# Performance work log

Measured on AMD Instinct MI355X. Metric: run time of the kernel, lower is better.

The kernel has to match this reference:

```python
import jax, jax.numpy as jnp
import numpy as np

B, T, D = 4, 2048, 768
D_CONV, D_GRIF, D_FFN, K = 384, 384, 2048, 3
EPS = 1e-6


def rmsnorm(x, w):
    rms = jax.lax.rsqrt(jnp.mean(jnp.square(x.astype(jnp.float32)), axis=-1, keepdims=True) + EPS)
    return (x.astype(jnp.float32) * rms).astype(x.dtype) * w


def causal_dwconv(x, w):
    # x: [B,T,C], w: [C,K] depthwise causal conv
    k = w.shape[1]
    xp = jnp.pad(x, ((0, 0), (k - 1, 0), (0, 0)))  # left pad -> causal
    out = jax.lax.conv_general_dilated(
        xp.transpose(0, 2, 1), w[:, None, :],  # [B,C,T+K-1], [C,1,K]
        window_strides=(1,), padding='VALID',
        dimension_numbers=('NCW', 'OIW', 'NCW'),
        feature_group_count=w.shape[0])
    return out.transpose(0, 2, 1)  # [B,T,C]


def rg_lru(v, r, i, lam):
    # Griffin RG-LRU: log_a = -8*softplus(lam)*r; h_t = a*h_{t-1} + sqrt(1-a^2)*(i*v)
    log_a = -8.0 * jax.nn.softplus(lam) * r                # [B,T,Dg]
    a = jnp.exp(log_a)
    gated = jnp.sqrt(jnp.maximum(1.0 - jnp.exp(2.0 * log_a), EPS)) * (i * v)
    def comb(c1, c2):
        a1, b1 = c1
        a2, b2 = c2
        return (a1 * a2, a2 * b1 + b2)
    _, h = jax.lax.associative_scan(comb, (a, gated), axis=1)
    return h


def setup_inputs() -> dict:
    key = jax.random.key(0)
    ks = jax.random.split(key, 16)
    s_in = 1.0 / np.sqrt(D)
    s_ffn = 1.0 / np.sqrt(D_FFN)
    return {
        'x': jax.random.normal(ks[0], (B, T, D), jnp.float32),
        'velocity': jnp.zeros((B, T, D), jnp.float32),
        'pre_norm_w': jnp.ones((D,), jnp.float32),
        'conv_in_w': jax.random.normal(ks[1], (D, 2 * D_CONV), jnp.float32) * s_in,
        'conv_dw_w': jax.random.normal(ks[2], (D_CONV, K), jnp.float32) * (1.0 / np.sqrt(K)),
        'grif_v_w': jax.random.normal(ks[3], (D, D_GRIF), jnp.float32) * s_in,
        'grif_r_w': jax.random.normal(ks[4], (D, D_GRIF), jnp.float32) * s_in,
        'grif_i_w': jax.random.normal(ks[5], (D, D_GRIF), jnp.float32) * s_in,
        'grif_lam': jax.random.uniform(ks[6], (D_GRIF,), jnp.float32, 0.5, 2.0),
        'out_w': jax.random.normal(ks[7], (D, D), jnp.float32) * s_in,
        'log_beta': jnp.array(0.0, jnp.float32),  # log(0.5/(1-0.5))
        'ffn_norm_w': jnp.ones((D,), jnp.float32),
        'w1': jax.random.normal(ks[8], (D, D_FFN), jnp.float32) * s_in,
        'w3': jax.random.normal(ks[9], (D, D_FFN), jnp.float32) * s_in,
        'w2': jax.random.normal(ks[10], (D_FFN, D), jnp.float32) * s_ffn,
    }


def reference(x, velocity, pre_norm_w, conv_in_w, conv_dw_w, grif_v_w, grif_r_w,
              grif_i_w, grif_lam, out_w, log_beta, ffn_norm_w, w1, w3, w2):
    xn = rmsnorm(x, pre_norm_w)
    # GatedConv branch -> [B,T,D_CONV]
    u, g = jnp.split(xn @ conv_in_w, 2, axis=-1)
    conv_out = causal_dwconv(u, conv_dw_w) * jax.nn.silu(g)
    # Griffin RG-LRU branch -> [B,T,D_GRIF]
    v = xn @ grif_v_w
    r = jax.nn.sigmoid(xn @ grif_r_w)
    i = jax.nn.sigmoid(xn @ grif_i_w)
    griffin_out = rg_lru(v, r, i, grif_lam)
    # concat -> out_proj -> momentum residual
    mixer_out = jnp.concatenate([conv_out, griffin_out], axis=-1) @ out_w
    beta = jax.nn.sigmoid(log_beta)
    velocity = beta * velocity + mixer_out
    x = x + velocity
    # ffn: RMSNorm -> SwiGLU -> residual
    normed = rmsnorm(x, ffn_norm_w)
    x = x + (jax.nn.silu(normed @ w1) * (normed @ w3)) @ w2
    return (x, velocity)
```

## Files before the change

kernel.cpp:

```cpp
#include <hip/hip_runtime.h>
#include <hip/hip_bf16.h>
#include <cstdint>

#define BSZ   4
#define TSEQ  2048
#define DMOD  768
#define DCONV 384
#define DGRIF 384
#define DFFN  2048
#define BT    (BSZ*TSEQ)
#define NG1   1920
#define EPS_  1e-6f

typedef __bf16 bf16;
typedef __bf16 bf16x8 __attribute__((ext_vector_type(8)));
typedef float  f32x4  __attribute__((ext_vector_type(4)));

__device__ __forceinline__ float sigmoidf_(float x) { return 1.f / (1.f + __expf(-x)); }

__device__ __forceinline__ void gload_lds16(const void* g, void* l) {
  __builtin_amdgcn_global_load_lds(
      (const __attribute__((address_space(1))) void*)(uintptr_t)g,
      (__attribute__((address_space(3))) void*)(uint32_t)(uintptr_t)l,
      16, 0, 0);
}

__device__ __forceinline__ int swz_wg() {
  const int nwg = gridDim.x;
  const int bid = blockIdx.x;
  const int cpx = nwg >> 3;
  return (bid & 7) * cpx + (bid >> 3);
}

__global__ __launch_bounds__(256) void prep_kernel(
    const float* __restrict__ conv_in_w, const float* __restrict__ gv,
    const float* __restrict__ gr, const float* __restrict__ gi,
    const float* __restrict__ out_w, const float* __restrict__ w1,
    const float* __restrict__ w3, const float* __restrict__ w2,
    bf16* __restrict__ WT_G1, bf16* __restrict__ WT_OUT,
    bf16* __restrict__ WT_W13, bf16* __restrict__ WT_W2,
    const float* __restrict__ x, const float* __restrict__ pre_w,
    bf16* __restrict__ XN)
{
  __shared__ float tile[32][33];
  if (blockIdx.x >= 6624) {
    const int row = blockIdx.x - 6624;
    const int tid = threadIdx.x;
    const float* xr = x + (size_t)row * DMOD;
    float v0 = xr[tid], v1 = xr[tid + 256], v2 = xr[tid + 512];
    float s = v0*v0 + v1*v1 + v2*v2;
    #pragma unroll
    for (int o = 32; o > 0; o >>= 1) s += __shfl_down(s, o, 64);
    __shared__ float sbuf[4];
    if ((tid & 63) == 0) sbuf[tid >> 6] = s;
    __syncthreads();
    float tot = sbuf[0] + sbuf[1] + sbuf[2] + sbuf[3];
    float rms = rsqrtf(tot * (1.f / (float)DMOD) + EPS_);
    bf16* orow = XN + (size_t)row * DMOD;
    orow[tid]       = (bf16)(v0 * rms * pre_w[tid]);
    orow[tid + 256] = (bf16)(v1 * rms * pre_w[tid + 256]);
    orow[tid + 512] = (bf16)(v2 * rms * pre_w[tid + 512]);
    return;
  }
  int t = blockIdx.x;
  const float* W; bf16* Wt; int R, C, mode = 0, half = 0;
  if      (t < 576)  {           W = conv_in_w; Wt = WT_G1;                        R = 768;  C = 768; }
  else if (t < 864)  { t -= 576;  W = gv;  Wt = WT_G1 + (size_t)768  * DMOD;       R = 768;  C = 384; }
  else if (t < 1152) { t -= 864;  W = gr;  Wt = WT_G1 + (size_t)1152 * DMOD;       R = 768;  C = 384; }
  else if (t < 1440) { t -= 1152; W = gi;  Wt = WT_G1 + (size_t)1536 * DMOD;       R = 768;  C = 384; }
  else if (t < 2016) { t -= 1440; W = out_w; Wt = WT_OUT;                          R = 768;  C = 768; }
  else if (t < 3552) { t -= 2016; W = w1;  Wt = WT_W13; mode = 1; half = 0;        R = 768;  C = 2048; }
  else if (t < 5088) { t -= 3552; W = w3;  Wt = WT_W13; mode = 1; half = 64;       R = 768;  C = 2048; }
  else               { t -= 5088; W = w2;  Wt = WT_W2;                             R = 2048; C = 768; }

  const int xt = C >> 5;
  const int tc = (t % xt) * 32, tr = (t / xt) * 32;
  const int lx = threadIdx.x & 31;
  const int ly = threadIdx.x >> 5;
  #pragma unroll
  for (int i = ly; i < 32; i += 8) {
    int r = tr + i, c = tc + lx;
    tile[i][lx] = (r < R && c < C) ? W[(size_t)r * C + c] : 0.f;
  }
  __syncthreads();
  #pragma unroll
  for (int i = ly; i < 32; i += 8) {
    int oc = tc + i;
    int orr = tr + lx;
    if (oc < C && orr < R) {
      int orow = (mode == 0) ? oc : ((oc >> 6) << 7) + half + (oc & 63);
      Wt[(size_t)orow * R + orr] = (bf16)tile[lx][i];
    }
  }
}

__global__ __launch_bounds__(256) void rmsnorm_kernel(
    const float* __restrict__ x, const float* __restrict__ w, bf16* __restrict__ out)
{
  __shared__ float sbuf[4];
  const int row = blockIdx.x;
  const int tid = threadIdx.x;
  const float* xr = x + (size_t)row * DMOD;
  float v0 = xr[tid], v1 = xr[tid + 256], v2 = xr[tid + 512];
  float s = v0*v0 + v1*v1 + v2*v2;
  #pragma unroll
  for (int o = 32; o > 0; o >>= 1) s += __shfl_down(s, o, 64);
  if ((tid & 63) == 0) sbuf[tid >> 6] = s;
  __syncthreads();
  float tot = sbuf[0] + sbuf[1] + sbuf[2] + sbuf[3];
  float rms = rsqrtf(tot * (1.f / (float)DMOD) + EPS_);
  bf16* orow = out + (size_t)row * DMOD;
  orow[tid]       = (bf16)(v0 * rms * w[tid]);
  orow[tid + 256] = (bf16)(v1 * rms * w[tid + 256]);
  orow[tid + 512] = (bf16)(v2 * rms * w[tid + 512]);
}

__global__ __launch_bounds__(256) void gemm_w128(
    const bf16* __restrict__ A, const bf16* __restrict__ Bt, bf16* __restrict__ C,
    int M, int N, int K, int nx)
{
  __shared__ alignas(16) unsigned short As[128 * 64];
  __shared__ alignas(16) unsigned short Bs[128 * 64];

  const int wg = swz_wg();
  const int m0 = (wg / nx) * 128, n0 = (wg % nx) * 128;
  const int tid  = threadIdx.x;
  const int wave = tid >> 6;
  const int lane = tid & 63;
  const int wr = wave >> 1, wc = wave & 1;

  f32x4 acc[4][4] = {};
  const int srow = lane >> 3;
  const int scol = ((lane & 7) ^ srow) * 8;
  const int lr = lane & 15;
  const int lsw = lr & 7;
  const int lk4 = lane >> 4;

  for (int k0 = 0; k0 < K; k0 += 64) {
    __syncthreads();
    #pragma unroll
    for (int it = 0; it < 4; ++it) {
      const int chunk = wave * 4 + it;
      const int row = chunk * 8 + srow;
      gload_lds16(A  + (size_t)(m0 + row) * K + k0 + scol, (char*)As + chunk * 1024);
      gload_lds16(Bt + (size_t)(n0 + row) * K + k0 + scol, (char*)Bs + chunk * 1024);
    }
    __syncthreads();
    #pragma unroll
    for (int kk = 0; kk < 2; ++kk) {
      bf16x8 af[4], bfr[4];
      #pragma unroll
      for (int i = 0; i < 4; ++i)
        af[i] = *reinterpret_cast<const bf16x8*>(
            &As[(wr*64 + i*16 + lr) * 64 + (((kk*4 + lk4) ^ lsw) * 8)]);
      #pragma unroll
      for (int i = 0; i < 4; ++i)
        bfr[i] = *reinterpret_cast<const bf16x8*>(
            &Bs[(wc*64 + i*16 + lr) * 64 + (((kk*4 + lk4) ^ lsw) * 8)]);
      #pragma unroll
      for (int mi = 0; mi < 4; ++mi)
        #pragma unroll
        for (int ni = 0; ni < 4; ++ni)
          acc[mi][ni] = __builtin_amdgcn_mfma_f32_16x16x32_bf16(af[mi], bfr[ni], acc[mi][ni], 0, 0, 0);
    }
  }

  #pragma unroll
  for (int mi = 0; mi < 4; ++mi)
    #pragma unroll
    for (int ni = 0; ni < 4; ++ni)
      #pragma unroll
      for (int reg = 0; reg < 4; ++reg) {
        const int r = m0 + wr*64 + mi*16 + lk4 * 4 + reg;
        const int c = n0 + wc*64 + ni*16 + lr;
        C[(size_t)r * N + c] = (bf16)acc[mi][ni][reg];
      }
}

__global__ __launch_bounds__(512) void gemm_ffn13b(
    const bf16* __restrict__ A, const bf16* __restrict__ Bt, bf16* __restrict__ H,
    int M, int K)
{
  __shared__ alignas(16) unsigned short As[256 * 64];
  __shared__ alignas(16) unsigned short Bs[128 * 64];
  bf16* comb = reinterpret_cast<bf16*>(As);

  const int xcd = blockIdx.x & 7;
  const int w   = blockIdx.x >> 3;
  const int mt  = (xcd & 3) * 8 + (w >> 4);
  const int bx  = (xcd >> 2) * 16 + (w & 15);
  const int m0 = mt * 256;
  const int n0 = bx * 128;
  const int tid  = threadIdx.x;
  const int wave = tid >> 6;
  const int lane = tid & 63;
  const int wr = wave >> 1;
  const int wc = wave & 1;
  const int lr = lane & 15;
  const int lk4 = lane >> 4;

  f32x4 acc[4][4] = {};

  for (int k0 = 0; k0 < K; k0 += 64) {
    __syncthreads();
    #pragma unroll
    for (int p = 0; p < 4; ++p) {
      const int f = (p << 9) + tid;
      const int row = f >> 3;
      const int gs = (f & 7) ^ (row & 7);
      gload_lds16(A + (size_t)(m0 + row) * K + k0 + gs * 8,
                  (char*)As + (p << 13) + (wave << 10));
    }
    #pragma unroll
    for (int p = 0; p < 2; ++p) {
      const int f = (p << 9) + tid;
      const int row = f >> 3;
      const int gs = (f & 7) ^ (row & 7);
      gload_lds16(Bt + (size_t)(n0 + row) * K + k0 + gs * 8,
                  (char*)Bs + (p << 13) + (wave << 10));
    }
    __syncthreads();
    #pragma unroll
    for (int kk = 0; kk < 2; ++kk) {
      bf16x8 af[4], bfr[4];
      #pragma unroll
      for (int i = 0; i < 4; ++i) {
        const int r = wr*64 + i*16 + lr;
        af[i] = *reinterpret_cast<const bf16x8*>(&As[r * 64 + (((kk*4 + lk4) ^ (r & 7)) * 8)]);
      }
      #pragma unroll
      for (int i = 0; i < 4; ++i) {
        const int r = wc*64 + i*16 + lr;
        bfr[i] = *reinterpret_cast<const bf16x8*>(&Bs[r * 64 + (((kk*4 + lk4) ^ (r & 7)) * 8)]);
      }
      #pragma unroll
      for (int mi = 0; mi < 4; ++mi)
        #pragma unroll
        for (int ni = 0; ni < 4; ++ni)
          acc[mi][ni] = __builtin_amdgcn_mfma_f32_16x16x32_bf16(af[mi], bfr[ni], acc[mi][ni], 0, 0, 0);
    }
  }

  __syncthreads();
  if (wc == 1) {
    #pragma unroll
    for (int mi = 0; mi < 4; ++mi)
      #pragma unroll
      for (int ni = 0; ni < 4; ++ni)
        #pragma unroll
        for (int reg = 0; reg < 4; ++reg) {
          const int row = wr*64 + mi*16 + lk4 * 4 + reg;
          const int col = ni*16 + lr;
          comb[row * 64 + col] = (bf16)acc[mi][ni][reg];
        }
  }
  __syncthreads();
  if (wc == 0) {
    #pragma unroll
    for (int mi = 0; mi < 4; ++mi)
      #pragma unroll
      for (int ni = 0; ni < 4; ++ni)
        #pragma unroll
        for (int reg = 0; reg < 4; ++reg) {
          const int row = wr*64 + mi*16 + lk4 * 4 + reg;
          const int col = ni*16 + lr;
          float p3 = (float)comb[row * 64 + col];
          float p1 = acc[mi][ni][reg];
          H[(size_t)(m0 + row) * DFFN + bx * 64 + col] = (bf16)(p1 * sigmoidf_(p1) * p3);
        }
  }
}

template <int EPI>
__global__ __launch_bounds__(256) void gemm_n64(
    const bf16* __restrict__ A, const bf16* __restrict__ Bt, float* __restrict__ C,
    const float* __restrict__ xin, const float* __restrict__ vin,
    float* __restrict__ outv, const float* __restrict__ log_beta,
    int M, int N, int K, int nx)
{
  __shared__ alignas(16) unsigned short As[2][128 * 64];
  __shared__ alignas(16) unsigned short Bs[2][64 * 64];

  const int wg = swz_wg();
  const int m0 = (wg / nx) * 128, n0 = (wg % nx) * 64;
  const int tid  = threadIdx.x;
  const int wave = tid >> 6;
  const int lane = tid & 63;
  const int wr = wave >> 1, wc = wave & 1;

  f32x4 acc[4][2] = {};
  const int srow = lane >> 3;
  const int scol = ((lane & 7) ^ srow) * 8;
  const int lr = lane & 15;
  const int lsw = lr & 7;
  const int lk4 = lane >> 4;

  auto stage = [&](int buf, int k0) {
    #pragma unroll
    for (int it = 0; it < 6; ++it) {
      const int chunk = wave * 6 + it;
      if (chunk < 16) {
        const int row = chunk * 8 + srow;
        gload_lds16(A + (size_t)(m0 + row) * K + k0 + scol,
                    (char*)As[buf] + chunk * 1024);
      } else {
        const int row = (chunk - 16) * 8 + srow;
        gload_lds16(Bt + (size_t)(n0 + row) * K + k0 + scol,
                    (char*)Bs[buf] + (chunk - 16) * 1024);
      }
    }
  };

  stage(0, 0);
  __syncthreads();

  int cur = 0;
  for (int k0 = 0; k0 < K; k0 += 64) {
    if (k0 + 64 < K) stage(cur ^ 1, k0 + 64);
    #pragma unroll
    for (int kk = 0; kk < 2; ++kk) {
      bf16x8 af[4], bfr[2];
      #pragma unroll
      for (int i = 0; i < 4; ++i)
        af[i] = *reinterpret_cast<const bf16x8*>(
            &As[cur][(wr*64 + i*16 + lr) * 64 + (((kk*4 + lk4) ^ lsw) * 8)]);
      #pragma unroll
      for (int i = 0; i < 2; ++i)
        bfr[i] = *reinterpret_cast<const bf16x8*>(
            &Bs[cur][(wc*32 + i*16 + lr) * 64 + (((kk*4 + lk4) ^ lsw) * 8)]);
      #pragma unroll
      for (int mi = 0; mi < 4; ++mi)
        #pragma unroll
        for (int ni = 0; ni < 2; ++ni)
          acc[mi][ni] = __builtin_amdgcn_mfma_f32_16x16x32_bf16(af[mi], bfr[ni], acc[mi][ni], 0, 0, 0);
    }
    __syncthreads();
    cur ^= 1;
  }

  const float beta = (EPI == 0) ? sigmoidf_(log_beta[0]) : 0.f;
  #pragma unroll
  for (int mi = 0; mi < 4; ++mi)
    #pragma unroll
    for (int ni = 0; ni < 2; ++ni)
      #pragma unroll
      for (int reg = 0; reg < 4; ++reg) {
        const int r = m0 + wr*64 + mi*16 + lk4 * 4 + reg;
        const int c = n0 + wc*32 + ni*16 + lr;
        const size_t off = (size_t)r * N + c;
        float v = acc[mi][ni][reg];
        if (EPI == 0) {
          float vel = beta * vin[off] + v;
          float x1  = xin[off] + vel;
          outv[off] = vel;
          C[off] = x1;
        } else {
          C[off] += v;
        }
      }
}

#define NCH  32
#define CLEN 64

__device__ __forceinline__ void lru_step(const bf16* row, int c, float coef,
                                         float& a, float& g)
{
  float v  = (float)row[2*DCONV + c];
  float r  = sigmoidf_((float)row[2*DCONV + DGRIF + c]);
  float is = sigmoidf_((float)row[2*DCONV + 2*DGRIF + c]);
  float la = coef * r;
  a = __expf(la);
  g = sqrtf(fmaxf(1.f - __expf(2.f * la), EPS_)) * (is * v);
}

__global__ __launch_bounds__(256) void lru_pass1(
    const bf16* __restrict__ g1, const float* __restrict__ lam,
    float* __restrict__ cA, float* __restrict__ cB)
{
  const int idx = blockIdx.x * 256 + threadIdx.x;
  const int c = idx % DGRIF;
  const int rest = idx / DGRIF;
  const int j = rest & (NCH - 1);
  const int b = rest / NCH;
  const float coef = -8.f * log1pf(__expf(lam[c]));
  const bf16* base = g1 + (size_t)(b * TSEQ + j * CLEN) * NG1;
  float A = 1.f, Bv = 0.f;
  #pragma unroll 4
  for (int t = 0; t < CLEN; ++t) {
    float a, g;
    lru_step(base + (size_t)t * NG1, c, coef, a, g);
    A *= a;
    Bv = a * Bv + g;
  }
  cA[((size_t)b * DGRIF + c) * NCH + j] = A;
  cB[((size_t)b * DGRIF + c) * NCH + j] = Bv;
}

__global__ __launch_bounds__(256) void lru_pass2(
    const bf16* __restrict__ g1, const float* __restrict__ lam,
    const float* __restrict__ cA, const float* __restrict__ cB,
    const float* __restrict__ dw, bf16* __restrict__ mixin)
{
  const int idx = blockIdx.x * 256 + threadIdx.x;
  const int c = idx % DGRIF;
  const int rest = idx / DGRIF;
  const int j = rest & (NCH - 1);
  const int b = rest / NCH;
  const float coef = -8.f * log1pf(__expf(lam[c]));
  float Hc = 0.f;
  const float* pa = cA + ((size_t)b * DGRIF + c) * NCH;
  const float* pb = cB + ((size_t)b * DGRIF + c) * NCH;
  for (int k = 0; k < j; ++k) Hc = pa[k] * Hc + pb[k];

  const int t0 = j * CLEN;
  const bf16* base = g1 + (size_t)(b * TSEQ + t0) * NG1;
  const float w0 = dw[c*3], w1 = dw[c*3 + 1], w2 = dw[c*3 + 2];
  float u1 = (t0 >= 1) ? (float)base[-(ptrdiff_t)NG1 + c]     : 0.f;
  float u0 = (t0 >= 2) ? (float)base[-(ptrdiff_t)(2*NG1) + c] : 0.f;

  bf16* mbase = mixin + (size_t)(b * TSEQ + t0) * DMOD;
  #pragma unroll 4
  for (int t = 0; t < CLEN; ++t) {
    const bf16* row = base + (size_t)t * NG1;
    float u2 = (float)row[c];
    float gg = (float)row[DCONV + c];
    float conv = u0 * w0 + u1 * w1 + u2 * w2;
    mbase[(size_t)t * DMOD + c] = (bf16)(conv * (gg * sigmoidf_(gg)));
    u0 = u1; u1 = u2;
    float a, g;
    lru_step(row, c, coef, a, g);
    Hc = a * Hc + g;
    mbase[(size_t)t * DMOD + DCONV + c] = (bf16)Hc;
  }
}

extern "C" void kernel_launch(void* const* d_in, const int* in_sizes, int n_in,
                              void* d_out, int out_size, void* d_ws, size_t ws_size,
                              hipStream_t stream)
{
  const float* x         = (const float*)d_in[0];
  const float* vel_in    = (const float*)d_in[1];
  const float* pre_w     = (const float*)d_in[2];
  const float* conv_in_w = (const float*)d_in[3];
  const float* conv_dw   = (const float*)d_in[4];
  const float* gv        = (const float*)d_in[5];
  const float* gr        = (const float*)d_in[6];
  const float* gi        = (const float*)d_in[7];
  const float* lam       = (const float*)d_in[8];
  const float* out_w     = (const float*)d_in[9];
  const float* log_beta  = (const float*)d_in[10];
  const float* ffn_w     = (const float*)d_in[11];
  const float* w1        = (const float*)d_in[12];
  const float* w3        = (const float*)d_in[13];
  const float* w2        = (const float*)d_in[14];

  char* ws = (char*)d_ws;
  size_t off = 0;
  auto alloc = [&](size_t bytes) { void* p = ws + off; off += (bytes + 255) & ~(size_t)255; return p; };

  bf16*  WT_G1  = (bf16*)alloc((size_t)NG1 * DMOD * 2);
  bf16*  WT_OUT = (bf16*)alloc((size_t)DMOD * DMOD * 2);
  bf16*  WT_W13 = (bf16*)alloc((size_t)2 * DFFN * DMOD * 2);
  bf16*  WT_W2  = (bf16*)alloc((size_t)DMOD * DFFN * 2);
  float* CA     = (float*)alloc((size_t)BSZ * DGRIF * NCH * 4);
  float* CB     = (float*)alloc((size_t)BSZ * DGRIF * NCH * 4);
  bf16*  XN     = (bf16*)alloc((size_t)BT * DMOD * 2);
  bf16*  G1     = (bf16*)alloc((size_t)BT * NG1 * 2);
  bf16*  MIXIN  = (bf16*)alloc((size_t)BT * DMOD * 2);
  bf16*  H      = (bf16*)alloc((size_t)BT * DFFN * 2);
  bf16*  NORMED = (bf16*)alloc((size_t)BT * DMOD * 2);

  float* OUTX   = (float*)d_out;
  float* OUTV   = OUTX + (size_t)BT * DMOD;

  prep_kernel<<<6624 + BT, 256, 0, stream>>>(conv_in_w, gv, gr, gi, out_w, w1, w3, w2,
                                             WT_G1, WT_OUT, WT_W13, WT_W2,
                                             x, pre_w, XN);

  gemm_w128<<<(NG1/128) * (BT/128), 256, 0, stream>>>(XN, WT_G1, G1, BT, NG1, DMOD, NG1/128);

  lru_pass1<<<(BSZ * NCH * DGRIF) / 256, 256, 0, stream>>>(G1, lam, CA, CB);
  lru_pass2<<<(BSZ * NCH * DGRIF) / 256, 256, 0, stream>>>(G1, lam, CA, CB, conv_dw, MIXIN);

  gemm_n64<0><<<(DMOD/64) * (BT/128), 256, 0, stream>>>(MIXIN, WT_OUT, OUTX, x, vel_in, OUTV,
                                                        log_beta, BT, DMOD, DMOD, DMOD/64);

  rmsnorm_kernel<<<BT, 256, 0, stream>>>(OUTX, ffn_w, NORMED);

  gemm_ffn13b<<<(BT/256) * (DFFN/64), 512, 0, stream>>>(NORMED, WT_W13, H, BT, DMOD);

  gemm_n64<1><<<(DMOD/64) * (BT/128), 256, 0, stream>>>(H, WT_W2, OUTX, nullptr, nullptr, nullptr,
                                                        nullptr, BT, DMOD, DFFN, DMOD/64);
}
```

Measured before the change: 259.9 us.

## Double-buffer LDS in input and FFN up-projection GEMMs, shrink FFN tile

Both the first projection GEMM and the fused W1/W3 GEMM now use two LDS buffers, so the tile for the next K step is fetched while MFMAs run on the current one. This halves the barriers per K step and aims to hide global-load latency. The FFN GEMM also moves from 256x128 tiles with 512 threads and a custom XCD mapping to 128x128 tiles with 256 threads and the shared swizzle, which gives more workgroups but less reuse per tile. LDS use doubles, which may lower occupancy.

```diff
diff --git a/kernel.cpp b/kernel.cpp
--- a/kernel.cpp
+++ b/kernel.cpp
@@ -115,12 +115,12 @@
   orow[tid + 512] = (bf16)(v2 * rms * w[tid + 512]);
 }
 
-__global__ __launch_bounds__(256) void gemm_w128(
+__global__ __launch_bounds__(256) void gemm_w128d(
     const bf16* __restrict__ A, const bf16* __restrict__ Bt, bf16* __restrict__ C,
     int M, int N, int K, int nx)
 {
-  __shared__ alignas(16) unsigned short As[128 * 64];
-  __shared__ alignas(16) unsigned short Bs[128 * 64];
+  __shared__ alignas(16) unsigned short As[2][128 * 64];
+  __shared__ alignas(16) unsigned short Bs[2][128 * 64];
 
   const int wg = swz_wg();
   const int m0 = (wg / nx) * 128, n0 = (wg % nx) * 128;
@@ -136,33 +136,41 @@
   const int lsw = lr & 7;
   const int lk4 = lane >> 4;
 
-  for (int k0 = 0; k0 < K; k0 += 64) {
-    __syncthreads();
+  auto stage = [&](int buf, int k0) {
     #pragma unroll
     for (int it = 0; it < 4; ++it) {
       const int chunk = wave * 4 + it;
       const int row = chunk * 8 + srow;
-      gload_lds16(A  + (size_t)(m0 + row) * K + k0 + scol, (char*)As + chunk * 1024);
-      gload_lds16(Bt + (size_t)(n0 + row) * K + k0 + scol, (char*)Bs + chunk * 1024);
-    }
-    __syncthreads();
+      gload_lds16(A  + (size_t)(m0 + row) * K + k0 + scol, (char*)As[buf] + chunk * 1024);
+      gload_lds16(Bt + (size_t)(n0 + row) * K + k0 + scol, (char*)Bs[buf] + chunk * 1024);
+    }
+  };
+
+  stage(0, 0);
+  __syncthreads();
+
+  int cur = 0;
+  for (int k0 = 0; k0 < K; k0 += 64) {
+    if (k0 + 64 < K) stage(cur ^ 1, k0 + 64);
     #pragma unroll
     for (int kk = 0; kk < 2; ++kk) {
       bf16x8 af[4], bfr[4];
       #pragma unroll
       for (int i = 0; i < 4; ++i)
         af[i] = *reinterpret_cast<const bf16x8*>(
-            &As[(wr*64 + i*16 + lr) * 64 + (((kk*4 + lk4) ^ lsw) * 8)]);
+            &As[cur][(wr*64 + i*16 + lr) * 64 + (((kk*4 + lk4) ^ lsw) * 8)]);
       #pragma unroll
       for (int i = 0; i < 4; ++i)
         bfr[i] = *reinterpret_cast<const bf16x8*>(
-            &Bs[(wc*64 + i*16 + lr) * 64 + (((kk*4 + lk4) ^ lsw) * 8)]);
+            &Bs[cur][(wc*64 + i*16 + lr) * 64 + (((kk*4 + lk4) ^ lsw) * 8)]);
       #pragma unroll
       for (int mi = 0; mi < 4; ++mi)
         #pragma unroll
         for (int ni = 0; ni < 4; ++ni)
           acc[mi][ni] = __builtin_amdgcn_mfma_f32_16x16x32_bf16(af[mi], bfr[ni], acc[mi][ni], 0, 0, 0);
     }
+    __syncthreads();
+    cur ^= 1;
   }
 
   #pragma unroll
@@ -177,71 +185,67 @@
       }
 }
 
-__global__ __launch_bounds__(512) void gemm_ffn13b(
+__global__ __launch_bounds__(256) void gemm_ffn13c(
     const bf16* __restrict__ A, const bf16* __restrict__ Bt, bf16* __restrict__ H,
-    int M, int K)
-{
-  __shared__ alignas(16) unsigned short As[256 * 64];
-  __shared__ alignas(16) unsigned short Bs[128 * 64];
+    int M, int K, int nx)
+{
+  __shared__ alignas(16) unsigned short As[2][128 * 64];
+  __shared__ alignas(16) unsigned short Bs[2][128 * 64];
   bf16* comb = reinterpret_cast<bf16*>(As);
 
-  const int xcd = blockIdx.x & 7;
-  const int w   = blockIdx.x >> 3;
-  const int mt  = (xcd & 3) * 8 + (w >> 4);
-  const int bx  = (xcd >> 2) * 16 + (w & 15);
-  const int m0 = mt * 256;
+  const int wg = swz_wg();
+  const int m0 = (wg / nx) * 128;
+  const int bx = wg % nx;
   const int n0 = bx * 128;
   const int tid  = threadIdx.x;
   const int wave = tid >> 6;
   const int lane = tid & 63;
-  const int wr = wave >> 1;
-  const int wc = wave & 1;
+  const int wr = wave >> 1, wc = wave & 1;
+
+  f32x4 acc[4][4] = {};
+  const int srow = lane >> 3;
+  const int scol = ((lane & 7) ^ srow) * 8;
   const int lr = lane & 15;
+  const int lsw = lr & 7;
   const int lk4 = lane >> 4;
 
-  f32x4 acc[4][4] = {};
-
+  auto stage = [&](int buf, int k0) {
+    #pragma unroll
+    for (int it = 0; it < 4; ++it) {
+      const int chunk = wave * 4 + it;
+      const int row = chunk * 8 + srow;
+      gload_lds16(A  + (size_t)(m0 + row) * K + k0 + scol, (char*)As[buf] + chunk * 1024);
+      gload_lds16(Bt + (size_t)(n0 + row) * K + k0 + scol, (char*)Bs[buf] + chunk * 1024);
+    }
+  };
+
+  stage(0, 0);
+  __syncthreads();
+
+  int cur = 0;
   for (int k0 = 0; k0 < K; k0 += 64) {
-    __syncthreads();
-    #pragma unroll
-    for (int p = 0; p < 4; ++p) {
-      const int f = (p << 9) + tid;
-      const int row = f >> 3;
-      const int gs = (f & 7) ^ (row & 7);
-      gload_lds16(A + (size_t)(m0 + row) * K + k0 + gs * 8,
-                  (char*)As + (p << 13) + (wave << 10));
-    }
-    #pragma unroll
-    for (int p = 0; p < 2; ++p) {
-      const int f = (p << 9) + tid;
-      const int row = f >> 3;
-      const int gs = (f & 7) ^ (row & 7);
-      gload_lds16(Bt + (size_t)(n0 + row) * K + k0 + gs * 8,
-                  (char*)Bs + (p << 13) + (wave << 10));
-    }
-    __syncthreads();
+    if (k0 + 64 < K) stage(cur ^ 1, k0 + 64);
     #pragma unroll
     for (int kk = 0; kk < 2; ++kk) {
       bf16x8 af[4], bfr[4];
       #pragma unroll
-      for (int i = 0; i < 4; ++i) {
-        const int r = wr*64 + i*16 + lr;
-        af[i] = *reinterpret_cast<const bf16x8*>(&As[r * 64 + (((kk*4 + lk4) ^ (r & 7)) * 8)]);
-      }
-      #pragma unroll
-      for (int i = 0; i < 4; ++i) {
-        const int r = wc*64 + i*16 + lr;
-        bfr[i] = *reinterpret_cast<const bf16x8*>(&Bs[r * 64 + (((kk*4 + lk4) ^ (r & 7)) * 8)]);
-      }
+      for (int i = 0; i < 4; ++i)
+        af[i] = *reinterpret_cast<const bf16x8*>(
+            &As[cur][(wr*64 + i*16 + lr) * 64 + (((kk*4 + lk4) ^ lsw) * 8)]);
+      #pragma unroll
+      for (int i = 0; i < 4; ++i)
+        bfr[i] = *reinterpret_cast<const bf16x8*>(
+            &Bs[cur][(wc*64 + i*16 + lr) * 64 + (((kk*4 + lk4) ^ lsw) * 8)]);
       #pragma unroll
       for (int mi = 0; mi < 4; ++mi)
         #pragma unroll
         for (int ni = 0; ni < 4; ++ni)
           acc[mi][ni] = __builtin_amdgcn_mfma_f32_16x16x32_bf16(af[mi], bfr[ni], acc[mi][ni], 0, 0, 0);
     }
-  }
-
-  __syncthreads();
+    __syncthreads();
+    cur ^= 1;
+  }
+
   if (wc == 1) {
     #pragma unroll
     for (int mi = 0; mi < 4; ++mi)
@@ -478,7 +482,7 @@
                                              WT_G1, WT_OUT, WT_W13, WT_W2,
                                              x, pre_w, XN);
 
-  gemm_w128<<<(NG1/128) * (BT/128), 256, 0, stream>>>(XN, WT_G1, G1, BT, NG1, DMOD, NG1/128);
+  gemm_w128d<<<(NG1/128) * (BT/128), 256, 0, stream>>>(XN, WT_G1, G1, BT, NG1, DMOD, NG1/128);
 
   lru_pass1<<<(BSZ * NCH * DGRIF) / 256, 256, 0, stream>>>(G1, lam, CA, CB);
   lru_pass2<<<(BSZ * NCH * DGRIF) / 256, 256, 0, stream>>>(G1, lam, CA, CB, conv_dw, MIXIN);
@@ -488,7 +492,7 @@
 
   rmsnorm_kernel<<<BT, 256, 0, stream>>>(OUTX, ffn_w, NORMED);
 
-  gemm_ffn13b<<<(BT/256) * (DFFN/64), 512, 0, stream>>>(NORMED, WT_W13, H, BT, DMOD);
+  gemm_ffn13c<<<(DFFN/64) * (BT/128), 256, 0, stream>>>(NORMED, WT_W13, H, BT, DMOD, DFFN/64);
 
   gemm_n64<1><<<(DMOD/64) * (BT/128), 256, 0, stream>>>(H, WT_W2, OUTX, nullptr, nullptr, nullptr,
                                                         nullptr, BT, DMOD, DFFN, DMOD/64);
```

After: 253.3 us. 1.03x faster.
